# Kernel optimization log

Measured on AMD Instinct MI355X. Metric: run time of the kernel, lower is better.

## Reference

```python
import jax, jax.numpy as jnp
import numpy as np
from jax import lax

N, L, D, P, H, QK, VP = 1, 512, 256, 128, 8, 8, 8
FIN = H * P + H * VP * 7 + H * 7  # 1528: pair + value-point + beta features


def _l2g(R, t, p):
    # local_to_global: q = R @ p + t, applied over flattened point dims
    s = p.shape
    p3 = p.reshape(s[0], s[1], -1, 3)
    q = jnp.einsum('nlij,nlmj->nlmi', R, p3) + t[:, :, None, :]
    return q.reshape(s)


def _g2l(R, t, q):
    # global_to_local: p = R^T @ (q - t)
    s = q.shape
    q3 = q.reshape(s[0], s[1], -1, 3)
    p = jnp.einsum('nlji,nlmj->nlmi', R, q3 - t[:, :, None, :])
    return p.reshape(s)


def _inorm(x):  # InstanceNorm2d, affine=False, eps=1e-5, NCHW
    m = x.mean(axis=(2, 3), keepdims=True)
    v = x.var(axis=(2, 3), keepdims=True)
    return (x - m) * lax.rsqrt(v + 1e-5)


def _conv3(x, w, b):  # 3x3, stride 1, pad 1
    y = lax.conv_general_dilated(x, w, (1, 1), [(1, 1), (1, 1)],
                                 dimension_numbers=('NCHW', 'OIHW', 'NCHW'))
    return y + b[None, :, None, None]


def _ln(x, g, b):  # LayerNorm over last dim, eps=1e-5
    m = x.mean(-1, keepdims=True)
    v = x.var(-1, keepdims=True)
    return (x - m) * lax.rsqrt(v + 1e-5) * g + b


def _leaky(x):  # LeakyReLU, negative_slope=0.01
    return jnp.where(x >= 0, x, 0.01 * x)


def setup_inputs():
    key = jax.random.key(0)
    ks = jax.random.split(key, 24)
    s = 0.05
    return {
        'R': jax.random.normal(ks[0], (N, L, 3, 3), jnp.float32),
        't': jax.random.normal(ks[1], (N, L, 3), jnp.float32),
        'p_CB': jax.random.normal(ks[2], (N, L, 3), jnp.float32),
        'x': jax.random.normal(ks[3], (N, L, D), jnp.float32),
        'z': jax.random.normal(ks[4], (N, L, L, P), jnp.float32),
        'W_p2h': jax.random.normal(ks[5], (P, H), jnp.float32) * s,
        'gamma': jnp.ones((1, 1, H), jnp.float32),
        'Wq': jax.random.normal(ks[6], (D, H * QK * 3), jnp.float32) * s,
        'Wk': jax.random.normal(ks[7], (D, H * QK * 3), jnp.float32) * s,
        'Wv': jax.random.normal(ks[8], (D, H * VP * 3), jnp.float32) * s,
        'W1': jax.random.normal(ks[9], (FIN, 2 * D), jnp.float32) * s,
        'b1': jnp.zeros((2 * D,), jnp.float32),
        'ln1_g': jnp.ones((2 * D,), jnp.float32),
        'ln1_b': jnp.zeros((2 * D,), jnp.float32),
        'W2': jax.random.normal(ks[10], (2 * D, D), jnp.float32) * s,
        'b2': jnp.zeros((D,), jnp.float32),
        'ca_w': jax.random.normal(ks[11], (H, 2 * H, 3, 3), jnp.float32) * s,
        'ca_b': jnp.zeros((H,), jnp.float32),
        'ln_g': jnp.ones((D,), jnp.float32),
        'ln_b': jnp.zeros((D,), jnp.float32),
        'cp_w': jax.random.normal(ks[12], (P, H + P, 3, 3), jnp.float32) * s,
        'cp_b': jnp.zeros((P,), jnp.float32),
        'mask': jnp.ones((N, L), dtype=bool),
    }


def reference(R, t, p_CB, x, z, W_p2h, gamma, Wq, Wk, Wv, W1, b1, ln1_g, ln1_b,
              W2, b2, ca_w, ca_b, ln_g, ln_b, cp_w, cp_b, mask):
    n, l = x.shape[:2]
    # pair logits [n,l,l,H]
    logits_pair = jnp.einsum('nijp,ph->nijh', z, W_p2h)
    # spatial (point) logits: squared distances between global q/k points
    q_s = _l2g(R, t, (x @ Wq).reshape(n, l, H * QK, 3)).reshape(n, l, H, QK * 3)
    k_s = _l2g(R, t, (x @ Wk).reshape(n, l, H * QK, 3)).reshape(n, l, H, QK * 3)
    ssd = ((q_s ** 2).sum(-1)[:, :, None, :] + (k_s ** 2).sum(-1)[:, None, :, :]
           - 2.0 * jnp.einsum('nihd,njhd->nijh', q_s, k_s))
    logits_spatial = ssd * (-gamma * jnp.sqrt(2.0 / (9.0 * QK)) / 2.0)
    # conv2dalpha: InstanceNorm -> 3x3 conv -> LeakyReLU over the LxL grid
    lg = jnp.concatenate([logits_pair, logits_spatial], axis=-1).transpose(0, 3, 1, 2)
    logits_sum = _leaky(_conv3(_inorm(lg), ca_w, ca_b)).transpose(0, 2, 3, 1)
    mask_row = mask[:, :, None, None]
    mask_pair = mask_row & mask[:, None, :, None]
    logits_sum = jnp.where(mask_pair, logits_sum, logits_sum - 1e6)
    alpha = jax.nn.softmax(logits_sum, axis=2)
    alpha = jnp.where(mask_row, alpha, 0.0)
    # pair aggregation [n,l,H*P]
    feat_p2n = jnp.einsum('nijh,nijp->nihp', alpha, z).reshape(n, l, H * P)
    # spatial (value point) aggregation
    v_pts = _l2g(R, t, (x @ Wv).reshape(n, l, H, VP, 3))
    aggr = jnp.einsum('nijh,njhvc->nihvc', alpha, v_pts)
    fp = _g2l(R, t, aggr)  # [n,l,H,VP,3]
    fn = jnp.sqrt((fp ** 2).sum(-1))
    fdir = fp / (fn[..., None] + 1e-6)
    feat_spatial = jnp.concatenate(
        [fp.reshape(n, l, -1), fn.reshape(n, l, -1), fdir.reshape(n, l, -1)], -1)
    # beta (CB point) aggregation
    aggr_b = jnp.einsum('nijh,njc->nihc', alpha, p_CB)
    fpb = _g2l(R, t, aggr_b)  # [n,l,H,3]
    fnb = jnp.sqrt((fpb ** 2).sum(-1))
    fdb = fpb / (fnb[..., None] + 1e-6)
    feat_beta = jnp.concatenate([fpb.reshape(n, l, -1), fnb, fdb.reshape(n, l, -1)], -1)
    # out_transform: Linear -> LayerNorm -> LeakyReLU -> Linear
    feat_all = jnp.concatenate([feat_p2n, feat_spatial, feat_beta], -1)
    h1 = _leaky(_ln(feat_all @ W1 + b1, ln1_g, ln1_b))
    fa = h1 @ W2 + b2
    fa = jnp.where(mask[..., None], fa, 0.0)
    x_out = _ln(x + fa, ln_g, ln_b)
    # alpha2pair: InstanceNorm -> 3x3 conv -> LeakyReLU
    pz = jnp.concatenate([z, alpha], -1).transpose(0, 3, 1, 2)
    pair_out = _leaky(_conv3(_inorm(pz), cp_w, cp_b)).transpose(0, 2, 3, 1)
    return (x_out, pair_out)
```

## Files before the change

kernel.cpp:

```cpp
#include <hip/hip_runtime.h>
#include <hip/hip_bf16.h>
#include <math.h>

#define Lr 512
#define LL (512*512)
#define PZROW 73728

typedef __bf16 bf16x8 __attribute__((ext_vector_type(8)));
typedef float f32x16 __attribute__((ext_vector_type(16)));

static __device__ __forceinline__ unsigned short f2bf(float f) {
    union { float f; unsigned u; } a; a.f = f;
    unsigned r = a.u + 0x7fff + ((a.u >> 16) & 1);
    return (unsigned short)(r >> 16);
}

static __device__ __forceinline__ unsigned pack2(float lo, float hi) {
    return (unsigned)f2bf(lo) | ((unsigned)f2bf(hi) << 16);
}

__global__ __launch_bounds__(512) void zero_stats_k(float* lg_acc, float* pz_acc) {
    int t = threadIdx.x;
    if (t < 32) lg_acc[t] = 0.f;
    if (t < 272) pz_acc[t] = 0.f;
}

__global__ __launch_bounds__(256) void wb_prep_k(const float* __restrict__ cpw,
        const float* __restrict__ pzmr, unsigned short* __restrict__ wb) {
    int idx = blockIdx.x * 256 + threadIdx.x;
    if (idx >= 128 * 1296) return;
    int o = idx / 1296, k = idx % 1296;
    int tap = k / 144, c = k % 144;
    float v = (c < 136) ? cpw[(o * 136 + c) * 9 + tap] * pzmr[c * 2 + 1] : 0.f;
    wb[idx] = f2bf(v);
}

__global__ __launch_bounds__(128) void kc_prep_k(const float* __restrict__ cpw,
        const float* __restrict__ pzmr, float* __restrict__ kc) {
    int idx = blockIdx.x * 128 + threadIdx.x;
    if (idx >= 1152) return;
    int o = idx / 9, tap = idx % 9;
    float s = 0.f;
    for (int c = 0; c < 136; c++)
        s += cpw[(o * 136 + c) * 9 + tap] * pzmr[c * 2 + 1] * pzmr[c * 2];
    kc[idx] = -s;
}

__device__ __forceinline__ const float* qkv_colptr(const float* Wq, const float* Wk, const float* Wv, int c) {
    return c < 192 ? (Wq + c) : (c < 384 ? (Wk + c - 192) : (Wv + c - 384));
}

__global__ __launch_bounds__(256) void qkv_k(const float* __restrict__ x,
        const float* __restrict__ Wq, const float* __restrict__ Wk, const float* __restrict__ Wv,
        const float* __restrict__ R, const float* __restrict__ tv,
        float* __restrict__ qs, float* __restrict__ ks, float* __restrict__ vp,
        float* __restrict__ q2, float* __restrict__ k2) {
    __shared__ float xrow[256];
    __shared__ float praw[576];
    __shared__ float tr[576];
    __shared__ float Rt[12];
    int i = blockIdx.x, t = threadIdx.x;
    xrow[t] = x[i * 256 + t];
    if (t < 12) Rt[t] = (t < 9) ? R[i * 9 + t] : tv[i * 3 + t - 9];
    __syncthreads();
    const float* p0 = qkv_colptr(Wq, Wk, Wv, t);
    const float* p1 = qkv_colptr(Wq, Wk, Wv, t + 256);
    const float* p2 = qkv_colptr(Wq, Wk, Wv, t < 64 ? t + 512 : 575);
    float a0 = 0.f, a1 = 0.f, a2 = 0.f;
    for (int f = 0; f < 256; f++) {
        float xv = xrow[f];
        a0 += xv * p0[f * 192];
        a1 += xv * p1[f * 192];
        a2 += xv * p2[f * 192];
    }
    praw[t] = a0; praw[t + 256] = a1;
    if (t < 64) praw[t + 512] = a2;
    __syncthreads();
    if (t < 192) {
        int seg = t / 64, pt = t % 64;
        float b0 = praw[seg * 192 + pt * 3], b1_ = praw[seg * 192 + pt * 3 + 1], b2_ = praw[seg * 192 + pt * 3 + 2];
        #pragma unroll
        for (int r = 0; r < 3; r++)
            tr[seg * 192 + pt * 3 + r] = Rt[r * 3] * b0 + Rt[r * 3 + 1] * b1_ + Rt[r * 3 + 2] * b2_ + Rt[9 + r];
    }
    __syncthreads();
    if (t < 8) {
        float s = 0.f;
        #pragma unroll
        for (int d = 0; d < 24; d++) { float v = tr[t * 24 + d]; s += v * v; }
        q2[i * 8 + t] = s;
    } else if (t < 16) {
        int h = t - 8; float s = 0.f;
        #pragma unroll
        for (int d = 0; d < 24; d++) { float v = tr[192 + h * 24 + d]; s += v * v; }
        k2[i * 8 + h] = s;
    }
    for (int f = t; f < 576; f += 256) {
        float v = tr[f];
        if (f < 192) qs[i * 192 + f] = v;
        else if (f < 384) ks[i * 192 + f - 192] = v;
        else vp[i * 192 + f - 384] = v;
    }
}

__global__ __launch_bounds__(256) void zstats_pzb_k(const float4* __restrict__ z4,
        float* pz_acc, unsigned short* __restrict__ pzb) {
    __shared__ float acc[256];
    int t = threadIdx.x;
    acc[t] = 0.f;
    __syncthreads();
    int chunk = t & 15, pl = t >> 4;
    int p0 = blockIdx.x * 128;
    float s[8], s2[8];
    #pragma unroll
    for (int u = 0; u < 8; u++) { s[u] = 0.f; s2[u] = 0.f; }
    #pragma unroll
    for (int k = 0; k < 8; k++) {
        int pos = p0 + k * 16 + pl;
        const float4* src = z4 + (size_t)pos * 32 + chunk * 2;
        float4 v0 = src[0], v1 = src[1];
        float vv[8] = {v0.x, v0.y, v0.z, v0.w, v1.x, v1.y, v1.z, v1.w};
        #pragma unroll
        for (int u = 0; u < 8; u++) { s[u] += vv[u]; s2[u] += vv[u] * vv[u]; }
        uint4 q;
        q.x = pack2(vv[0], vv[1]); q.y = pack2(vv[2], vv[3]);
        q.z = pack2(vv[4], vv[5]); q.w = pack2(vv[6], vv[7]);
        int row = pos >> 9, col = pos & 511;
        *(uint4*)(pzb + ((size_t)row * 18 + chunk) * 4096 + col * 8) = q;
    }
    #pragma unroll
    for (int u = 0; u < 8; u++) {
        atomicAdd(&acc[(chunk * 8 + u) * 2], s[u]);
        atomicAdd(&acc[(chunk * 8 + u) * 2 + 1], s2[u]);
    }
    __syncthreads();
    if (t < 128) {
        atomicAdd(&pz_acc[t * 2], acc[t * 2]);
        atomicAdd(&pz_acc[t * 2 + 1], acc[t * 2 + 1]);
    }
}

__global__ __launch_bounds__(256) void lg_k(const float* __restrict__ z,
        const float* __restrict__ Wp2h, const float* __restrict__ gamma,
        const float* __restrict__ qs, const float* __restrict__ ks,
        const float* __restrict__ q2, const float* __restrict__ k2,
        float* __restrict__ lg, float* lg_acc) {
    __shared__ float zl[32 * 132];
    __shared__ float wh[8 * 132];
    __shared__ float qrow[192];
    __shared__ float q2row[8];
    __shared__ float sacc[32];
    int i = blockIdx.x, t = threadIdx.x;
    for (int f = t; f < 1024; f += 256) { int h = f >> 7, p = f & 127; wh[h * 132 + p] = Wp2h[p * 8 + h]; }
    if (t < 192) qrow[t] = qs[i * 192 + t];
    if (t < 8) q2row[t] = q2[i * 8 + t];
    if (t < 32) sacc[t] = 0.f;
    int jl = t >> 3, h = t & 7;
    float gsc = -gamma[h] * 0.08333333333333333f;
    float sp = 0.f, sp2 = 0.f, ss = 0.f, ss2 = 0.f;
    __syncthreads();
    for (int jt = 0; jt < 16; jt++) {
        int j0 = jt * 32;
        const float4* zsrc = (const float4*)(z + (size_t)(i * 512 + j0) * 128);
        #pragma unroll
        for (int r = 0; r < 4; r++) {
            int idx4 = r * 256 + t;
            int zjl = idx4 >> 5, p4 = idx4 & 31;
            *(float4*)&zl[zjl * 132 + p4 * 4] = zsrc[idx4];
        }
        __syncthreads();
        int j = j0 + jl;
        float accp = 0.f;
        const float4* za = (const float4*)&zl[jl * 132];
        const float4* wa = (const float4*)&wh[h * 132];
        #pragma unroll
        for (int p4 = 0; p4 < 32; p4++) {
            float4 a = za[p4], b = wa[p4];
            accp += a.x * b.x + a.y * b.y + a.z * b.z + a.w * b.w;
        }
        const float4* kp = (const float4*)(ks + (size_t)j * 192 + h * 24);
        const float4* qp = (const float4*)&qrow[h * 24];
        float dqk = 0.f;
        #pragma unroll
        for (int d4 = 0; d4 < 6; d4++) {
            float4 a = qp[d4], b = kp[d4];
            dqk += a.x * b.x + a.y * b.y + a.z * b.z + a.w * b.w;
        }
        float ssd = q2row[h] + k2[j * 8 + h] - 2.f * dqk;
        float lgs = ssd * gsc;
        lg[(size_t)h * LL + i * 512 + j] = accp;
        lg[(size_t)(8 + h) * LL + i * 512 + j] = lgs;
        sp += accp; sp2 += accp * accp; ss += lgs; ss2 += lgs * lgs;
        __syncthreads();
    }
    atomicAdd(&sacc[h * 2], sp);        atomicAdd(&sacc[h * 2 + 1], sp2);
    atomicAdd(&sacc[16 + h * 2], ss);   atomicAdd(&sacc[16 + h * 2 + 1], ss2);
    __syncthreads();
    if (t < 16) {
        atomicAdd(&lg_acc[t * 2], sacc[t * 2]);
        atomicAdd(&lg_acc[t * 2 + 1], sacc[t * 2 + 1]);
    }
}

__global__ void finalize_k(const float* __restrict__ acc, float* __restrict__ mr, int nch, float npix) {
    int t = threadIdx.x;
    if (t < nch) {
        float m = acc[t * 2] / npix;
        float v = acc[t * 2 + 1] / npix - m * m;
        mr[t * 2] = m;
        mr[t * 2 + 1] = rsqrtf(fmaxf(v, 0.f) + 1e-5f);
    }
}

__global__ __launch_bounds__(256) void ca_softmax_k(const float* __restrict__ lg,
        const float* __restrict__ lgmr, const float* __restrict__ caw, const float* __restrict__ cab,
        float* __restrict__ alpha, float* pz_acc, unsigned short* __restrict__ pzb) {
    __shared__ float wl[1152];
    __shared__ float mr[32];
    __shared__ float cb[8];
    __shared__ float red[64];
    int i = blockIdx.x, t = threadIdx.x;
    for (int f = t; f < 1152; f += 256) {
        int o = f & 7, k = f >> 3; int c = k / 9, r = k % 9;
        wl[f] = caw[(o * 16 + c) * 9 + r];
    }
    if (t < 32) mr[t] = lgmr[t];
    if (t < 8) cb[t] = cab[t];
    __syncthreads();
    float acc0[8], acc1[8];
    #pragma unroll
    for (int o = 0; o < 8; o++) { acc0[o] = 0.f; acc1[o] = 0.f; }
    int j0 = t, j1 = t + 256;
    const float4* w4 = (const float4*)wl;
    for (int c = 0; c < 16; c++) {
        float m = mr[c * 2], rs = mr[c * 2 + 1];
        const float* lgc = lg + (size_t)c * LL;
        #pragma unroll
        for (int di = 0; di < 3; di++) {
            int row = i - 1 + di;
            if (row < 0 || row >= 512) continue;
            const float* lr = lgc + (size_t)row * 512;
            float v0[3], v1[3];
            v0[0] = (j0 > 0) ? (lr[j0 - 1] - m) * rs : 0.f;
            v0[1] = (lr[j0] - m) * rs;
            v0[2] = (lr[j0 + 1] - m) * rs;
            v1[0] = (lr[j1 - 1] - m) * rs;
            v1[1] = (lr[j1] - m) * rs;
            v1[2] = (j1 < 511) ? (lr[j1 + 1] - m) * rs : 0.f;
            int wb = (c * 9 + di * 3) * 2;
            #pragma unroll
            for (int dj = 0; dj < 3; dj++) {
                float4 wa = w4[wb + dj * 2], wbv = w4[wb + dj * 2 + 1];
                acc0[0] += wa.x * v0[dj]; acc0[1] += wa.y * v0[dj]; acc0[2] += wa.z * v0[dj]; acc0[3] += wa.w * v0[dj];
                acc0[4] += wbv.x * v0[dj]; acc0[5] += wbv.y * v0[dj]; acc0[6] += wbv.z * v0[dj]; acc0[7] += wbv.w * v0[dj];
                acc1[0] += wa.x * v1[dj]; acc1[1] += wa.y * v1[dj]; acc1[2] += wa.z * v1[dj]; acc1[3] += wa.w * v1[dj];
                acc1[4] += wbv.x * v1[dj]; acc1[5] += wbv.y * v1[dj]; acc1[6] += wbv.z * v1[dj]; acc1[7] += wbv.w * v1[dj];
            }
        }
    }
    float s0[8], s1[8];
    #pragma unroll
    for (int o = 0; o < 8; o++) {
        float v = acc0[o] + cb[o]; s0[o] = v >= 0.f ? v : 0.01f * v;
        float w = acc1[o] + cb[o]; s1[o] = w >= 0.f ? w : 0.01f * w;
    }
    int lane = t & 63, wid = t >> 6;
    float mx[8];
    #pragma unroll
    for (int o = 0; o < 8; o++) mx[o] = fmaxf(s0[o], s1[o]);
    for (int off = 1; off < 64; off <<= 1) {
        #pragma unroll
        for (int o = 0; o < 8; o++) mx[o] = fmaxf(mx[o], __shfl_xor(mx[o], off));
    }
    if (lane == 0) {
        #pragma unroll
        for (int o = 0; o < 8; o++) red[wid * 8 + o] = mx[o];
    }
    __syncthreads();
    float M[8];
    #pragma unroll
    for (int o = 0; o < 8; o++) M[o] = fmaxf(fmaxf(red[o], red[8 + o]), fmaxf(red[16 + o], red[24 + o]));
    float e0[8], e1[8], sm[8];
    #pragma unroll
    for (int o = 0; o < 8; o++) { e0[o] = expf(s0[o] - M[o]); e1[o] = expf(s1[o] - M[o]); sm[o] = e0[o] + e1[o]; }
    __syncthreads();
    for (int off = 1; off < 64; off <<= 1) {
        #pragma unroll
        for (int o = 0; o < 8; o++) sm[o] += __shfl_xor(sm[o], off);
    }
    if (lane == 0) {
        #pragma unroll
        for (int o = 0; o < 8; o++) red[wid * 8 + o] = sm[o];
    }
    __syncthreads();
    float a0[8], a1[8], st_s[8], st_q[8];
    #pragma unroll
    for (int o = 0; o < 8; o++) {
        float rden = 1.f / (red[o] + red[8 + o] + red[16 + o] + red[24 + o]);
        a0[o] = e0[o] * rden; a1[o] = e1[o] * rden;
        st_s[o] = a0[o] + a1[o];
        st_q[o] = a0[o] * a0[o] + a1[o] * a1[o];
    }
    size_t base = (size_t)i * 512;
    #pragma unroll
    for (int o = 0; o < 8; o++) {
        alpha[(size_t)o * LL + base + t] = a0[o];
        alpha[(size_t)o * LL + base + t + 256] = a1[o];
    }
    {
        uint4 p0, p1;
        p0.x = pack2(a0[0], a0[1]); p0.y = pack2(a0[2], a0[3]);
        p0.z = pack2(a0[4], a0[5]); p0.w = pack2(a0[6], a0[7]);
        p1.x = pack2(a1[0], a1[1]); p1.y = pack2(a1[2], a1[3]);
        p1.z = pack2(a1[4], a1[5]); p1.w = pack2(a1[6], a1[7]);
        unsigned short* pb = pzb + (size_t)i * PZROW + 16 * 4096;
        *(uint4*)(pb + (size_t)t * 8) = p0;
        *(uint4*)(pb + (size_t)(t + 256) * 8) = p1;
        uint4 zz = {0u, 0u, 0u, 0u};
        *(uint4*)(pb + 4096 + (size_t)t * 8) = zz;
        *(uint4*)(pb + 4096 + (size_t)(t + 256) * 8) = zz;
    }
    __syncthreads();
    for (int off = 1; off < 64; off <<= 1) {
        #pragma unroll
        for (int o = 0; o < 8; o++) { st_s[o] += __shfl_xor(st_s[o], off); st_q[o] += __shfl_xor(st_q[o], off); }
    }
    if (lane == 0) {
        #pragma unroll
        for (int o = 0; o < 8; o++) { red[wid * 8 + o] = st_s[o]; red[32 + wid * 8 + o] = st_q[o]; }
    }
    __syncthreads();
    if (t < 8) {
        float ts = red[t] + red[8 + t] + red[16 + t] + red[24 + t];
        float tq = red[32 + t] + red[40 + t] + red[48 + t] + red[56 + t];
        atomicAdd(&pz_acc[(128 + t) * 2], ts);
        atomicAdd(&pz_acc[(128 + t) * 2 + 1], tq);
    }
}

__global__ __launch_bounds__(256) void feat_mlp_k(
        const float* __restrict__ alpha, const float* __restrict__ z,
        const float* __restrict__ vp, const float* __restrict__ pcb,
        const float* __restrict__ R, const float* __restrict__ tv,
        const float* __restrict__ W1, const float* __restrict__ b1,
        const float* __restrict__ ln1g, const float* __restrict__ ln1b,
        const float* __restrict__ W2, const float* __restrict__ b2,
        const float* __restrict__ lng, const float* __restrict__ lnb,
        const float* __restrict__ x, float* __restrict__ xout) {
    __shared__ float al[8 * 512];
    __shared__ float zl[64 * 128];
    __shared__ float feat[1536];
    __shared__ float h1[512];
    __shared__ float agg[216];
    __shared__ float Rt[12];
    __shared__ float redl[8];
    int i = blockIdx.x, t = threadIdx.x;
    for (int f = t; f < 4096; f += 256) al[f] = alpha[(size_t)(f >> 9) * LL + i * 512 + (f & 511)];
    if (t < 12) Rt[t] = (t < 9) ? R[i * 9 + t] : tv[i * 3 + t - 9];
    __syncthreads();
    if (t < 216) {
        float a = 0.f;
        if (t < 192) {
            int h = t / 24;
            const float* vptr = vp + t;
            const float* ar = al + h * 512;
            for (int j = 0; j < 512; j++) a += ar[j] * vptr[(size_t)j * 192];
        } else {
            int u = t - 192; int h = u / 3, cc = u % 3;
            const float* ar = al + h * 512;
            for (int j = 0; j < 512; j++) a += ar[j] * pcb[j * 3 + cc];
        }
        agg[t] = a;
    }
    float4 accp = {0.f, 0.f, 0.f, 0.f};
    int hh = t >> 5, p4 = t & 31;
    for (int jc = 0; jc < 8; jc++) {
        const float4* zsrc = (const float4*)(z + (size_t)(i * 512 + jc * 64) * 128);
        #pragma unroll
        for (int r = 0; r < 8; r++) ((float4*)zl)[r * 256 + t] = zsrc[r * 256 + t];
        __syncthreads();
        const float* ar = al + hh * 512 + jc * 64;
        const float4* zv = (const float4*)zl + p4;
        #pragma unroll 4
        for (int jl = 0; jl < 64; jl++) {
            float a = ar[jl];
            float4 v = zv[jl * 32];
            accp.x += a * v.x; accp.y += a * v.y; accp.z += a * v.z; accp.w += a * v.w;
        }
        __syncthreads();
    }
    *(float4*)&feat[hh * 128 + p4 * 4] = accp;
    __syncthreads();
    if (t < 64) {
        int h = t >> 3, v = t & 7;
        float d0 = agg[h * 24 + v * 3] - Rt[9];
        float d1 = agg[h * 24 + v * 3 + 1] - Rt[10];
        float d2 = agg[h * 24 + v * 3 + 2] - Rt[11];
        float f0 = Rt[0] * d0 + Rt[3] * d1 + Rt[6] * d2;
        float f1 = Rt[1] * d0 + Rt[4] * d1 + Rt[7] * d2;
        float f2 = Rt[2] * d0 + Rt[5] * d1 + Rt[8] * d2;
        float n = sqrtf(f0 * f0 + f1 * f1 + f2 * f2);
        float rn = 1.f / (n + 1e-6f);
        feat[1024 + h * 24 + v * 3] = f0;
        feat[1024 + h * 24 + v * 3 + 1] = f1;
        feat[1024 + h * 24 + v * 3 + 2] = f2;
        feat[1216 + h * 8 + v] = n;
        feat[1280 + h * 24 + v * 3] = f0 * rn;
        feat[1280 + h * 24 + v * 3 + 1] = f1 * rn;
        feat[1280 + h * 24 + v * 3 + 2] = f2 * rn;
    } else if (t < 72) {
        int h = t - 64;
        float d0 = agg[192 + h * 3] - Rt[9];
        float d1 = agg[192 + h * 3 + 1] - Rt[10];
        float d2 = agg[192 + h * 3 + 2] - Rt[11];
        float f0 = Rt[0] * d0 + Rt[3] * d1 + Rt[6] * d2;
        float f1 = Rt[1] * d0 + Rt[4] * d1 + Rt[7] * d2;
        float f2 = Rt[2] * d0 + Rt[5] * d1 + Rt[8] * d2;
        float n = sqrtf(f0 * f0 + f1 * f1 + f2 * f2);
        float rn = 1.f / (n + 1e-6f);
        feat[1472 + h * 3] = f0; feat[1472 + h * 3 + 1] = f1; feat[1472 + h * 3 + 2] = f2;
        feat[1496 + h] = n;
        feat[1504 + h * 3] = f0 * rn; feat[1504 + h * 3 + 1] = f1 * rn; feat[1504 + h * 3 + 2] = f2 * rn;
    }
    __syncthreads();
    float acc0 = b1[t], acc1 = b1[t + 256];
    const float4* f4 = (const float4*)feat;
    for (int f = 0; f < 1528; f += 4) {
        float4 fv = f4[f >> 2];
        const float* w = W1 + (size_t)f * 512 + t;
        acc0 += fv.x * w[0] + fv.y * w[512] + fv.z * w[1024] + fv.w * w[1536];
        const float* w2p = w + 256;
        acc1 += fv.x * w2p[0] + fv.y * w2p[512] + fv.z * w2p[1024] + fv.w * w2p[1536];
    }
    int lane = t & 63, wid = t >> 6;
    float s = acc0 + acc1, s2 = acc0 * acc0 + acc1 * acc1;
    for (int off = 1; off < 64; off <<= 1) { s += __shfl_xor(s, off); s2 += __shfl_xor(s2, off); }
    if (lane == 0) { redl[wid * 2] = s; redl[wid * 2 + 1] = s2; }
    __syncthreads();
    float S = redl[0] + redl[2] + redl[4] + redl[6];
    float S2 = redl[1] + redl[3] + redl[5] + redl[7];
    float mean = S / 512.f;
    float rstd = rsqrtf(fmaxf(S2 / 512.f - mean * mean, 0.f) + 1e-5f);
    float hv0 = (acc0 - mean) * rstd * ln1g[t] + ln1b[t];
    float hv1 = (acc1 - mean) * rstd * ln1g[t + 256] + ln1b[t + 256];
    hv0 = hv0 >= 0.f ? hv0 : 0.01f * hv0;
    hv1 = hv1 >= 0.f ? hv1 : 0.01f * hv1;
    h1[t] = hv0; h1[t + 256] = hv1;
    __syncthreads();
    float a2 = b2[t];
    const float4* h14 = (const float4*)h1;
    for (int k = 0; k < 512; k += 4) {
        float4 hv = h14[k >> 2];
        const float* w = W2 + (size_t)k * 256 + t;
        a2 += hv.x * w[0] + hv.y * w[256] + hv.z * w[512] + hv.w * w[768];
    }
    float xv = x[i * 256 + t] + a2;
    float ss_ = xv, sq_ = xv * xv;
    for (int off = 1; off < 64; off <<= 1) { ss_ += __shfl_xor(ss_, off); sq_ += __shfl_xor(sq_, off); }
    __syncthreads();
    if (lane == 0) { redl[wid * 2] = ss_; redl[wid * 2 + 1] = sq_; }
    __syncthreads();
    float Sx = redl[0] + redl[2] + redl[4] + redl[6];
    float Sx2 = redl[1] + redl[3] + redl[5] + redl[7];
    float mx = Sx / 256.f;
    float rsx = rsqrtf(fmaxf(Sx2 / 256.f - mx * mx, 0.f) + 1e-5f);
    xout[i * 256 + t] = (xv - mx) * rsx * lng[t] + lnb[t];
}

__global__ __launch_bounds__(256) void conv_mfma_k(
        const unsigned short* __restrict__ pzb, const unsigned short* __restrict__ wb,
        const float* __restrict__ kc, const float* __restrict__ cpb,
        float* __restrict__ pout) {
    __shared__ unsigned short abuf[2368 * 8];
    __shared__ float csA[128];
    __shared__ float cs0[128];
    __shared__ float cs2[128];
    int t = threadIdx.x;
    int bid = blockIdx.x;
    int swz = (bid & 7) * 256 + (bid >> 3);
    int i = swz >> 2;
    int j0 = (swz & 3) * 128;
    if (t < 128) {
        int o = t;
        float a0 = 0.f, a1 = 0.f, a2 = 0.f;
        #pragma unroll
        for (int di = 0; di < 3; di++) {
            int grow = i - 1 + di;
            if (grow < 0 || grow > 511) continue;
            a0 += kc[o * 9 + di * 3];
            a1 += kc[o * 9 + di * 3 + 1];
            a2 += kc[o * 9 + di * 3 + 2];
        }
        cs0[o] = a0; cs2[o] = a2; csA[o] = cpb[o] + a0 + a1 + a2;
    }
    int w = t >> 6, lane = t & 63;
    int l31 = lane & 31, lhi = lane >> 5;
    int mt0 = (w & 1) * 64;
    int nt0 = (w >> 1) * 64;

    uint4 rg[10];
    #define STAGE_LOAD(DI) do {                                                \
        int grow_ = i - 1 + (DI);                                              \
        bool rowok_ = (grow_ >= 0 && grow_ < 512);                             \
        const unsigned short* rowp_ = pzb + (size_t)grow_ * PZROW;             \
        _Pragma("unroll")                                                      \
        for (int k = 0; k < 10; k++) {                                         \
            int f_ = t + k * 256;                                              \
            uint4 v_ = {0u, 0u, 0u, 0u};                                       \
            if (f_ < 2340) {                                                   \
                int c_ = f_ / 130, col_ = f_ - c_ * 130;                       \
                int gcol_ = j0 - 1 + col_;                                     \
                if (rowok_ && (unsigned)gcol_ < 512u)                          \
                    v_ = *(const uint4*)(rowp_ + c_ * 4096 + gcol_ * 8);       \
            }                                                                  \
            rg[k] = v_;                                                        \
        }                                                                      \
    } while (0)

    #define STAGE_WRITE() do {                                                 \
        _Pragma("unroll")                                                      \
        for (int k = 0; k < 10; k++) {                                         \
            int f_ = t + k * 256;                                              \
            if (f_ < 2340) *(uint4*)(abuf + f_ * 8) = rg[k];                   \
        }                                                                      \
    } while (0)

    f32x16 acc00 = {}, acc01 = {}, acc10 = {}, acc11 = {};

    STAGE_LOAD(0);
    STAGE_WRITE();
    __syncthreads();

    #pragma unroll
    for (int di = 0; di < 3; di++) {
        if (di < 2) STAGE_LOAD(di + 1);
        #pragma unroll
        for (int dj = 0; dj < 3; dj++) {
            int tap = di * 3 + dj;
            const unsigned short* wp0 = wb + (size_t)(nt0 + l31) * 1296 + tap * 144 + lhi * 8;
            const unsigned short* wp1 = wp0 + 32 * 1296;
            const unsigned short* ap0 = abuf + lhi * 1040 + (mt0 + l31 + dj) * 8;
            const unsigned short* ap1 = ap0 + 256;
            #pragma unroll
            for (int ksn = 0; ksn < 9; ksn++) {
                bf16x8 a0 = *(const bf16x8*)(ap0 + ksn * 2080);
                bf16x8 a1 = *(const bf16x8*)(ap1 + ksn * 2080);
                bf16x8 b0 = *(const bf16x8*)(wp0 + ksn * 16);
                bf16x8 b1 = *(const bf16x8*)(wp1 + ksn * 16);
                acc00 = __builtin_amdgcn_mfma_f32_32x32x16_bf16(a0, b0, acc00, 0, 0, 0);
                acc01 = __builtin_amdgcn_mfma_f32_32x32x16_bf16(a0, b1, acc01, 0, 0, 0);
                acc10 = __builtin_amdgcn_mfma_f32_32x32x16_bf16(a1, b0, acc10, 0, 0, 0);
                acc11 = __builtin_amdgcn_mfma_f32_32x32x16_bf16(a1, b1, acc11, 0, 0, 0);
            }
        }
        __syncthreads();
        if (di < 2) {
            STAGE_WRITE();
            __syncthreads();
        }
    }
    #undef STAGE_LOAD
    #undef STAGE_WRITE

    #pragma unroll
    for (int mi = 0; mi < 2; mi++) {
        #pragma unroll
        for (int ni = 0; ni < 2; ni++) {
            const f32x16* a = (mi == 0) ? (ni == 0 ? &acc00 : &acc01) : (ni == 0 ? &acc10 : &acc11);
            int nb = nt0 + ni * 32 + l31;
            float bA = csA[nb], b0_ = cs0[nb], b2_ = cs2[nb];
            #pragma unroll
            for (int r = 0; r < 16; r++) {
                int m = mt0 + mi * 32 + 4 * lhi + (r & 3) + 8 * (r >> 2);
                int j = j0 + m;
                float bias = bA - (j == 0 ? b0_ : 0.f) - (j == 511 ? b2_ : 0.f);
                float v = (*a)[r] + bias;
                v = v >= 0.f ? v : 0.01f * v;
                pout[((size_t)(i * 512 + j)) * 128 + nb] = v;
            }
        }
    }
}

extern "C" void kernel_launch(void* const* d_in, const int* in_sizes, int n_in,
                              void* d_out, int out_size, void* d_ws, size_t ws_size,
                              hipStream_t stream) {
    (void)in_sizes; (void)n_in; (void)out_size; (void)ws_size;
    const float* R    = (const float*)d_in[0];
    const float* tv   = (const float*)d_in[1];
    const float* pcb  = (const float*)d_in[2];
    const float* x    = (const float*)d_in[3];
    const float* z    = (const float*)d_in[4];
    const float* wp2h = (const float*)d_in[5];
    const float* gamma= (const float*)d_in[6];
    const float* Wq   = (const float*)d_in[7];
    const float* Wk   = (const float*)d_in[8];
    const float* Wv   = (const float*)d_in[9];
    const float* W1   = (const float*)d_in[10];
    const float* b1   = (const float*)d_in[11];
    const float* ln1g = (const float*)d_in[12];
    const float* ln1b = (const float*)d_in[13];
    const float* W2   = (const float*)d_in[14];
    const float* b2   = (const float*)d_in[15];
    const float* caw  = (const float*)d_in[16];
    const float* cab  = (const float*)d_in[17];
    const float* lng  = (const float*)d_in[18];
    const float* lnb  = (const float*)d_in[19];
    const float* cpw  = (const float*)d_in[20];
    const float* cpb  = (const float*)d_in[21];

    float* ws = (float*)d_ws;
    float* qs     = ws;
    float* ksv    = qs + 98304;
    float* vp     = ksv + 98304;
    float* q2     = vp + 98304;
    float* k2     = q2 + 4096;
    float* lg_acc = k2 + 4096;
    float* lg_mr  = lg_acc + 32;
    float* pz_acc = lg_mr + 32;
    float* pz_mr  = pz_acc + 272;
    float* kc     = pz_mr + 272;
    unsigned short* wbq = (unsigned short*)(kc + 1152);
    float* lg     = kc + 1152 + 82944;
    float* alpha  = lg + 16 * LL;
    unsigned short* pzb = (unsigned short*)(alpha + 8 * LL);

    float* xout = (float*)d_out;
    float* pout = xout + 131072;

    hipLaunchKernelGGL(zero_stats_k, dim3(1), dim3(512), 0, stream, lg_acc, pz_acc);
    hipLaunchKernelGGL(qkv_k, dim3(512), dim3(256), 0, stream, x, Wq, Wk, Wv, R, tv, qs, ksv, vp, q2, k2);
    hipLaunchKernelGGL(zstats_pzb_k, dim3(2048), dim3(256), 0, stream, (const float4*)z, pz_acc, pzb);
    hipLaunchKernelGGL(lg_k, dim3(512), dim3(256), 0, stream, z, wp2h, gamma, qs, ksv, q2, k2, lg, lg_acc);
    hipLaunchKernelGGL(finalize_k, dim3(1), dim3(64), 0, stream, lg_acc, lg_mr, 16, 262144.f);
    hipLaunchKernelGGL(ca_softmax_k, dim3(512), dim3(256), 0, stream, lg, lg_mr, caw, cab, alpha, pz_acc, pzb);
    hipLaunchKernelGGL(finalize_k, dim3(1), dim3(192), 0, stream, pz_acc, pz_mr, 136, 262144.f);
    hipLaunchKernelGGL(wb_prep_k, dim3(648), dim3(256), 0, stream, cpw, pz_mr, wbq);
    hipLaunchKernelGGL(kc_prep_k, dim3(9), dim3(128), 0, stream, cpw, pz_mr, kc);
    hipLaunchKernelGGL(feat_mlp_k, dim3(512), dim3(256), 0, stream,
                       alpha, z, vp, pcb, R, tv, W1, b1, ln1g, ln1b, W2, b2, lng, lnb, x, xout);
    hipLaunchKernelGGL(conv_mfma_k, dim3(2048), dim3(256), 0, stream, pzb, wbq, kc, cpb, pout);
}
```

Baseline: 775.0 us.

## Split feature aggregation from MLP, transpose value points, stage conv output stores

Measured after the change: 827.9 us. 1.07x slower.

```diff
diff --git a/kernel.cpp b/kernel.cpp
--- a/kernel.cpp
+++ b/kernel.cpp
@@ -19,10 +19,14 @@
     return (unsigned)f2bf(lo) | ((unsigned)f2bf(hi) << 16);
 }
 
-__global__ __launch_bounds__(512) void zero_stats_k(float* lg_acc, float* pz_acc) {
-    int t = threadIdx.x;
-    if (t < 32) lg_acc[t] = 0.f;
-    if (t < 272) pz_acc[t] = 0.f;
+__global__ __launch_bounds__(512) void zero_stats_k(float* lg_acc, float* pz_acc,
+        float* vpT, const float* __restrict__ pcb) {
+    int t = threadIdx.x, b = blockIdx.x;
+    if (b == 0) {
+        if (t < 32) lg_acc[t] = 0.f;
+        if (t < 272) pz_acc[t] = 0.f;
+    }
+    vpT[(size_t)(192 + b) * 512 + t] = pcb[t * 3 + b];
 }
 
 __global__ __launch_bounds__(256) void wb_prep_k(const float* __restrict__ cpw,
@@ -53,7 +57,7 @@
 __global__ __launch_bounds__(256) void qkv_k(const float* __restrict__ x,
         const float* __restrict__ Wq, const float* __restrict__ Wk, const float* __restrict__ Wv,
         const float* __restrict__ R, const float* __restrict__ tv,
-        float* __restrict__ qs, float* __restrict__ ks, float* __restrict__ vp,
+        float* __restrict__ qs, float* __restrict__ ks, float* __restrict__ vpT,
         float* __restrict__ q2, float* __restrict__ k2) {
     __shared__ float xrow[256];
     __shared__ float praw[576];
@@ -95,12 +99,12 @@
         for (int d = 0; d < 24; d++) { float v = tr[192 + h * 24 + d]; s += v * v; }
         k2[i * 8 + h] = s;
     }
-    for (int f = t; f < 576; f += 256) {
+    for (int f = t; f < 384; f += 256) {
         float v = tr[f];
         if (f < 192) qs[i * 192 + f] = v;
-        else if (f < 384) ks[i * 192 + f - 192] = v;
-        else vp[i * 192 + f - 384] = v;
-    }
+        else ks[i * 192 + f - 192] = v;
+    }
+    if (t < 192) vpT[(size_t)t * 512 + i] = tr[384 + t];
 }
 
 __global__ __launch_bounds__(256) void zstats_pzb_k(const float4* __restrict__ z4,
@@ -338,58 +342,61 @@
     }
 }
 
-__global__ __launch_bounds__(256) void feat_mlp_k(
+__global__ __launch_bounds__(256) void aggfeat_k(
         const float* __restrict__ alpha, const float* __restrict__ z,
-        const float* __restrict__ vp, const float* __restrict__ pcb,
+        const float* __restrict__ vpT,
         const float* __restrict__ R, const float* __restrict__ tv,
-        const float* __restrict__ W1, const float* __restrict__ b1,
-        const float* __restrict__ ln1g, const float* __restrict__ ln1b,
-        const float* __restrict__ W2, const float* __restrict__ b2,
-        const float* __restrict__ lng, const float* __restrict__ lnb,
-        const float* __restrict__ x, float* __restrict__ xout) {
+        float* __restrict__ featg) {
     __shared__ float al[8 * 512];
-    __shared__ float zl[64 * 128];
-    __shared__ float feat[1536];
-    __shared__ float h1[512];
+    __shared__ float zl[32 * 128];
     __shared__ float agg[216];
+    __shared__ float featl[512];
     __shared__ float Rt[12];
-    __shared__ float redl[8];
     int i = blockIdx.x, t = threadIdx.x;
-    for (int f = t; f < 4096; f += 256) al[f] = alpha[(size_t)(f >> 9) * LL + i * 512 + (f & 511)];
+    float4 rg[4];
+    const float4* zsrc = (const float4*)(z + (size_t)i * 512 * 128);
+    #pragma unroll
+    for (int k = 0; k < 4; k++) rg[k] = zsrc[k * 256 + t];
+    #pragma unroll
+    for (int f = t; f < 1024; f += 256)
+        ((float4*)al)[f] = ((const float4*)(alpha + (size_t)(f >> 7) * LL + (size_t)i * 512))[f & 127];
     if (t < 12) Rt[t] = (t < 9) ? R[i * 9 + t] : tv[i * 3 + t - 9];
-    __syncthreads();
-    if (t < 216) {
-        float a = 0.f;
-        if (t < 192) {
-            int h = t / 24;
-            const float* vptr = vp + t;
-            const float* ar = al + h * 512;
-            for (int j = 0; j < 512; j++) a += ar[j] * vptr[(size_t)j * 192];
-        } else {
-            int u = t - 192; int h = u / 3, cc = u % 3;
-            const float* ar = al + h * 512;
-            for (int j = 0; j < 512; j++) a += ar[j] * pcb[j * 3 + cc];
-        }
-        agg[t] = a;
-    }
+    int hh = t >> 5, p4 = t & 31;
     float4 accp = {0.f, 0.f, 0.f, 0.f};
-    int hh = t >> 5, p4 = t & 31;
-    for (int jc = 0; jc < 8; jc++) {
-        const float4* zsrc = (const float4*)(z + (size_t)(i * 512 + jc * 64) * 128);
-        #pragma unroll
-        for (int r = 0; r < 8; r++) ((float4*)zl)[r * 256 + t] = zsrc[r * 256 + t];
+    for (int jc = 0; jc < 16; jc++) {
+        #pragma unroll
+        for (int k = 0; k < 4; k++) ((float4*)zl)[k * 256 + t] = rg[k];
         __syncthreads();
-        const float* ar = al + hh * 512 + jc * 64;
+        if (jc < 15) {
+            const float4* zn = zsrc + (size_t)(jc + 1) * 1024;
+            #pragma unroll
+            for (int k = 0; k < 4; k++) rg[k] = zn[k * 256 + t];
+        }
+        const float* ar = al + hh * 512 + jc * 32;
         const float4* zv = (const float4*)zl + p4;
-        #pragma unroll 4
-        for (int jl = 0; jl < 64; jl++) {
+        #pragma unroll 8
+        for (int jl = 0; jl < 32; jl++) {
             float a = ar[jl];
             float4 v = zv[jl * 32];
             accp.x += a * v.x; accp.y += a * v.y; accp.z += a * v.z; accp.w += a * v.w;
         }
         __syncthreads();
     }
-    *(float4*)&feat[hh * 128 + p4 * 4] = accp;
+    *(float4*)(featg + (size_t)i * 1536 + t * 4) = accp;
+    if (t < 216) {
+        const float* src; int h;
+        if (t < 192) { src = vpT + (size_t)t * 512; h = t / 24; }
+        else { int u = t - 192; src = vpT + (size_t)(192 + u % 3) * 512; h = u / 3; }
+        const float4* s4 = (const float4*)src;
+        const float4* a4 = (const float4*)(al + h * 512);
+        float acc = 0.f;
+        #pragma unroll 8
+        for (int k = 0; k < 128; k++) {
+            float4 a = a4[k], b = s4[k];
+            acc += a.x * b.x + a.y * b.y + a.z * b.z + a.w * b.w;
+        }
+        agg[t] = acc;
+    }
     __syncthreads();
     if (t < 64) {
         int h = t >> 3, v = t & 7;
@@ -401,13 +408,13 @@
         float f2 = Rt[2] * d0 + Rt[5] * d1 + Rt[8] * d2;
         float n = sqrtf(f0 * f0 + f1 * f1 + f2 * f2);
         float rn = 1.f / (n + 1e-6f);
-        feat[1024 + h * 24 + v * 3] = f0;
-        feat[1024 + h * 24 + v * 3 + 1] = f1;
-        feat[1024 + h * 24 + v * 3 + 2] = f2;
-        feat[1216 + h * 8 + v] = n;
-        feat[1280 + h * 24 + v * 3] = f0 * rn;
-        feat[1280 + h * 24 + v * 3 + 1] = f1 * rn;
-        feat[1280 + h * 24 + v * 3 + 2] = f2 * rn;
+        featl[h * 24 + v * 3] = f0;
+        featl[h * 24 + v * 3 + 1] = f1;
+        featl[h * 24 + v * 3 + 2] = f2;
+        featl[192 + h * 8 + v] = n;
+        featl[256 + h * 24 + v * 3] = f0 * rn;
+        featl[256 + h * 24 + v * 3 + 1] = f1 * rn;
+        featl[256 + h * 24 + v * 3 + 2] = f2 * rn;
     } else if (t < 72) {
         int h = t - 64;
         float d0 = agg[192 + h * 3] - Rt[9];
@@ -418,53 +425,92 @@
         float f2 = Rt[2] * d0 + Rt[5] * d1 + Rt[8] * d2;
         float n = sqrtf(f0 * f0 + f1 * f1 + f2 * f2);
         float rn = 1.f / (n + 1e-6f);
-        feat[1472 + h * 3] = f0; feat[1472 + h * 3 + 1] = f1; feat[1472 + h * 3 + 2] = f2;
-        feat[1496 + h] = n;
-        feat[1504 + h * 3] = f0 * rn; feat[1504 + h * 3 + 1] = f1 * rn; feat[1504 + h * 3 + 2] = f2 * rn;
-    }
-    __syncthreads();
-    float acc0 = b1[t], acc1 = b1[t + 256];
-    const float4* f4 = (const float4*)feat;
-    for (int f = 0; f < 1528; f += 4) {
-        float4 fv = f4[f >> 2];
-        const float* w = W1 + (size_t)f * 512 + t;
-        acc0 += fv.x * w[0] + fv.y * w[512] + fv.z * w[1024] + fv.w * w[1536];
-        const float* w2p = w + 256;
-        acc1 += fv.x * w2p[0] + fv.y * w2p[512] + fv.z * w2p[1024] + fv.w * w2p[1536];
+        featl[448 + h * 3] = f0; featl[448 + h * 3 + 1] = f1; featl[448 + h * 3 + 2] = f2;
+        featl[472 + h] = n;
+        featl[480 + h * 3] = f0 * rn; featl[480 + h * 3 + 1] = f1 * rn; featl[480 + h * 3 + 2] = f2 * rn;
+    } else if (t < 80) {
+        featl[432 + t] = 0.f;
+    }
+    __syncthreads();
+    if (t < 128)
+        ((float4*)(featg + (size_t)i * 1536 + 1024))[t] = ((const float4*)featl)[t];
+}
+
+__global__ __launch_bounds__(256) void mlp_k(
+        const float* __restrict__ featg,
+        const float* __restrict__ W1, const float* __restrict__ b1,
+        const float* __restrict__ ln1g, const float* __restrict__ ln1b,
+        const float* __restrict__ W2, const float* __restrict__ b2,
+        const float* __restrict__ lng, const float* __restrict__ lnb,
+        const float* __restrict__ x, float* __restrict__ xout) {
+    __shared__ float fl[2][1528];
+    __shared__ float h1[2][512];
+    __shared__ float red[16];
+    int b = blockIdx.x, t = threadIdx.x;
+    int i0 = b * 2;
+    for (int f = t; f < 764; f += 256) {
+        int r = f / 382, k = f - r * 382;
+        ((float4*)fl[r])[k] = ((const float4*)(featg + (size_t)(i0 + r) * 1536))[k];
+    }
+    __syncthreads();
+    float a00 = b1[t], a01 = b1[t + 256];
+    float a10 = a00, a11 = a01;
+    for (int k = 0; k < 1528; k += 4) {
+        float4 f0 = *(const float4*)&fl[0][k];
+        float4 f1 = *(const float4*)&fl[1][k];
+        const float* w = W1 + (size_t)k * 512 + t;
+        float w0 = w[0], w1 = w[512], w2 = w[1024], w3 = w[1536];
+        float v0 = w[256], v1 = w[768], v2 = w[1280], v3 = w[1792];
+        a00 += f0.x * w0 + f0.y * w1 + f0.z * w2 + f0.w * w3;
+        a01 += f0.x * v0 + f0.y * v1 + f0.z * v2 + f0.w * v3;
+        a10 += f1.x * w0 + f1.y * w1 + f1.z * w2 + f1.w * w3;
+        a11 += f1.x * v0 + f1.y * v1 + f1.z * v2 + f1.w * v3;
     }
     int lane = t & 63, wid = t >> 6;
-    float s = acc0 + acc1, s2 = acc0 * acc0 + acc1 * acc1;
-    for (int off = 1; off < 64; off <<= 1) { s += __shfl_xor(s, off); s2 += __shfl_xor(s2, off); }
-    if (lane == 0) { redl[wid * 2] = s; redl[wid * 2 + 1] = s2; }
-    __syncthreads();
-    float S = redl[0] + redl[2] + redl[4] + redl[6];
-    float S2 = redl[1] + redl[3] + redl[5] + redl[7];
-    float mean = S / 512.f;
-    float rstd = rsqrtf(fmaxf(S2 / 512.f - mean * mean, 0.f) + 1e-5f);
-    float hv0 = (acc0 - mean) * rstd * ln1g[t] + ln1b[t];
-    float hv1 = (acc1 - mean) * rstd * ln1g[t + 256] + ln1b[t + 256];
-    hv0 = hv0 >= 0.f ? hv0 : 0.01f * hv0;
-    hv1 = hv1 >= 0.f ? hv1 : 0.01f * hv1;
-    h1[t] = hv0; h1[t + 256] = hv1;
-    __syncthreads();
-    float a2 = b2[t];
-    const float4* h14 = (const float4*)h1;
+    float s0 = a00 + a01, q0 = a00 * a00 + a01 * a01;
+    float s1 = a10 + a11, q1 = a10 * a10 + a11 * a11;
+    for (int off = 1; off < 64; off <<= 1) {
+        s0 += __shfl_xor(s0, off); q0 += __shfl_xor(q0, off);
+        s1 += __shfl_xor(s1, off); q1 += __shfl_xor(q1, off);
+    }
+    if (lane == 0) { red[wid * 4] = s0; red[wid * 4 + 1] = q0; red[wid * 4 + 2] = s1; red[wid * 4 + 3] = q1; }
+    __syncthreads();
+    float S0 = red[0] + red[4] + red[8] + red[12], Q0 = red[1] + red[5] + red[9] + red[13];
+    float S1 = red[2] + red[6] + red[10] + red[14], Q1 = red[3] + red[7] + red[11] + red[15];
+    float m0 = S0 / 512.f, r0 = rsqrtf(fmaxf(Q0 / 512.f - m0 * m0, 0.f) + 1e-5f);
+    float m1 = S1 / 512.f, r1 = rsqrtf(fmaxf(Q1 / 512.f - m1 * m1, 0.f) + 1e-5f);
+    float g0 = ln1g[t], g1 = ln1g[t + 256], bb0 = ln1b[t], bb1 = ln1b[t + 256];
+    float h00 = (a00 - m0) * r0 * g0 + bb0; h00 = h00 >= 0.f ? h00 : 0.01f * h00;
+    float h01 = (a01 - m0) * r0 * g1 + bb1; h01 = h01 >= 0.f ? h01 : 0.01f * h01;
+    float h10 = (a10 - m1) * r1 * g0 + bb0; h10 = h10 >= 0.f ? h10 : 0.01f * h10;
+    float h11 = (a11 - m1) * r1 * g1 + bb1; h11 = h11 >= 0.f ? h11 : 0.01f * h11;
+    h1[0][t] = h00; h1[0][t + 256] = h01; h1[1][t] = h10; h1[1][t + 256] = h11;
+    __syncthreads();
+    float c0 = b2[t], c1 = c0;
     for (int k = 0; k < 512; k += 4) {
-        float4 hv = h14[k >> 2];
+        float4 hv0 = *(const float4*)&h1[0][k];
+        float4 hv1 = *(const float4*)&h1[1][k];
         const float* w = W2 + (size_t)k * 256 + t;
-        a2 += hv.x * w[0] + hv.y * w[256] + hv.z * w[512] + hv.w * w[768];
-    }
-    float xv = x[i * 256 + t] + a2;
-    float ss_ = xv, sq_ = xv * xv;
-    for (int off = 1; off < 64; off <<= 1) { ss_ += __shfl_xor(ss_, off); sq_ += __shfl_xor(sq_, off); }
-    __syncthreads();
-    if (lane == 0) { redl[wid * 2] = ss_; redl[wid * 2 + 1] = sq_; }
-    __syncthreads();
-    float Sx = redl[0] + redl[2] + redl[4] + redl[6];
-    float Sx2 = redl[1] + redl[3] + redl[5] + redl[7];
-    float mx = Sx / 256.f;
-    float rsx = rsqrtf(fmaxf(Sx2 / 256.f - mx * mx, 0.f) + 1e-5f);
-    xout[i * 256 + t] = (xv - mx) * rsx * lng[t] + lnb[t];
+        float w0 = w[0], w1 = w[256], w2 = w[512], w3 = w[768];
+        c0 += hv0.x * w0 + hv0.y * w1 + hv0.z * w2 + hv0.w * w3;
+        c1 += hv1.x * w0 + hv1.y * w1 + hv1.z * w2 + hv1.w * w3;
+    }
+    float xv0 = x[(size_t)i0 * 256 + t] + c0;
+    float xv1 = x[(size_t)(i0 + 1) * 256 + t] + c1;
+    float ss0 = xv0, qq0 = xv0 * xv0, ss1 = xv1, qq1 = xv1 * xv1;
+    for (int off = 1; off < 64; off <<= 1) {
+        ss0 += __shfl_xor(ss0, off); qq0 += __shfl_xor(qq0, off);
+        ss1 += __shfl_xor(ss1, off); qq1 += __shfl_xor(qq1, off);
+    }
+    __syncthreads();
+    if (lane == 0) { red[wid * 4] = ss0; red[wid * 4 + 1] = qq0; red[wid * 4 + 2] = ss1; red[wid * 4 + 3] = qq1; }
+    __syncthreads();
+    float Sx0 = red[0] + red[4] + red[8] + red[12], Qx0 = red[1] + red[5] + red[9] + red[13];
+    float Sx1 = red[2] + red[6] + red[10] + red[14], Qx1 = red[3] + red[7] + red[11] + red[15];
+    float mx0 = Sx0 / 256.f, rx0 = rsqrtf(fmaxf(Qx0 / 256.f - mx0 * mx0, 0.f) + 1e-5f);
+    float mx1 = Sx1 / 256.f, rx1 = rsqrtf(fmaxf(Qx1 / 256.f - mx1 * mx1, 0.f) + 1e-5f);
+    xout[(size_t)i0 * 256 + t] = (xv0 - mx0) * rx0 * lng[t] + lnb[t];
+    xout[(size_t)(i0 + 1) * 256 + t] = (xv1 - mx1) * rx1 * lng[t] + lnb[t];
 }
 
 __global__ __launch_bounds__(256) void conv_mfma_k(
@@ -562,23 +608,38 @@
     #undef STAGE_LOAD
     #undef STAGE_WRITE
 
-    #pragma unroll
-    for (int mi = 0; mi < 2; mi++) {
-        #pragma unroll
-        for (int ni = 0; ni < 2; ni++) {
-            const f32x16* a = (mi == 0) ? (ni == 0 ? &acc00 : &acc01) : (ni == 0 ? &acc10 : &acc11);
-            int nb = nt0 + ni * 32 + l31;
-            float bA = csA[nb], b0_ = cs0[nb], b2_ = cs2[nb];
+    float* fb = (float*)abuf;
+    #pragma unroll
+    for (int mh = 0; mh < 2; mh++) {
+        if ((w & 1) == mh) {
             #pragma unroll
-            for (int r = 0; r < 16; r++) {
-                int m = mt0 + mi * 32 + 4 * lhi + (r & 3) + 8 * (r >> 2);
-                int j = j0 + m;
-                float bias = bA - (j == 0 ? b0_ : 0.f) - (j == 511 ? b2_ : 0.f);
-                float v = (*a)[r] + bias;
-                v = v >= 0.f ? v : 0.01f * v;
-                pout[((size_t)(i * 512 + j)) * 128 + nb] = v;
+            for (int mi = 0; mi < 2; mi++) {
+                #pragma unroll
+                for (int ni = 0; ni < 2; ni++) {
+                    const f32x16* a = (mi == 0) ? (ni == 0 ? &acc00 : &acc01) : (ni == 0 ? &acc10 : &acc11);
+                    int nb = nt0 + ni * 32 + l31;
+                    float bA = csA[nb], b0_ = cs0[nb], b2_ = cs2[nb];
+                    #pragma unroll
+                    for (int r = 0; r < 16; r++) {
+                        int ml = mi * 32 + 4 * lhi + (r & 3) + 8 * (r >> 2);
+                        int j = j0 + mh * 64 + ml;
+                        float bias = bA - (j == 0 ? b0_ : 0.f) - (j == 511 ? b2_ : 0.f);
+                        float v = (*a)[r] + bias;
+                        v = v >= 0.f ? v : 0.01f * v;
+                        fb[ml * 128 + nb] = v;
+                    }
+                }
             }
         }
+        __syncthreads();
+        const float4* fb4 = (const float4*)fb;
+        float4* gdst = (float4*)(pout + ((size_t)(i * 512 + j0 + mh * 64)) * 128);
+        #pragma unroll
+        for (int k = 0; k < 8; k++) {
+            int f4i = k * 256 + t;
+            gdst[f4i] = fb4[f4i];
+        }
+        __syncthreads();
     }
 }
 
@@ -612,8 +673,8 @@
     float* ws = (float*)d_ws;
     float* qs     = ws;
     float* ksv    = qs + 98304;
-    float* vp     = ksv + 98304;
-    float* q2     = vp + 98304;
+    float* vpT    = ksv + 98304;
+    float* q2     = vpT + 100352;
     float* k2     = q2 + 4096;
     float* lg_acc = k2 + 4096;
     float* lg_mr  = lg_acc + 32;
@@ -621,15 +682,16 @@
     float* pz_mr  = pz_acc + 272;
     float* kc     = pz_mr + 272;
     unsigned short* wbq = (unsigned short*)(kc + 1152);
-    float* lg     = kc + 1152 + 82944;
+    float* featg  = kc + 1152 + 82944;
+    float* lg     = featg + 786432;
     float* alpha  = lg + 16 * LL;
     unsigned short* pzb = (unsigned short*)(alpha + 8 * LL);
 
     float* xout = (float*)d_out;
     float* pout = xout + 131072;
 
-    hipLaunchKernelGGL(zero_stats_k, dim3(1), dim3(512), 0, stream, lg_acc, pz_acc);
-    hipLaunchKernelGGL(qkv_k, dim3(512), dim3(256), 0, stream, x, Wq, Wk, Wv, R, tv, qs, ksv, vp, q2, k2);
+    hipLaunchKernelGGL(zero_stats_k, dim3(3), dim3(512), 0, stream, lg_acc, pz_acc, vpT, pcb);
+    hipLaunchKernelGGL(qkv_k, dim3(512), dim3(256), 0, stream, x, Wq, Wk, Wv, R, tv, qs, ksv, vpT, q2, k2);
     hipLaunchKernelGGL(zstats_pzb_k, dim3(2048), dim3(256), 0, stream, (const float4*)z, pz_acc, pzb);
     hipLaunchKernelGGL(lg_k, dim3(512), dim3(256), 0, stream, z, wp2h, gamma, qs, ksv, q2, k2, lg, lg_acc);
     hipLaunchKernelGGL(finalize_k, dim3(1), dim3(64), 0, stream, lg_acc, lg_mr, 16, 262144.f);
@@ -637,7 +699,8 @@
     hipLaunchKernelGGL(finalize_k, dim3(1), dim3(192), 0, stream, pz_acc, pz_mr, 136, 262144.f);
     hipLaunchKernelGGL(wb_prep_k, dim3(648), dim3(256), 0, stream, cpw, pz_mr, wbq);
     hipLaunchKernelGGL(kc_prep_k, dim3(9), dim3(128), 0, stream, cpw, pz_mr, kc);
-    hipLaunchKernelGGL(feat_mlp_k, dim3(512), dim3(256), 0, stream,
-                       alpha, z, vp, pcb, R, tv, W1, b1, ln1g, ln1b, W2, b2, lng, lnb, x, xout);
+    hipLaunchKernelGGL(aggfeat_k, dim3(512), dim3(256), 0, stream, alpha, z, vpT, R, tv, featg);
+    hipLaunchKernelGGL(mlp_k, dim3(256), dim3(256), 0, stream,
+                       featg, W1, b1, ln1g, ln1b, W2, b2, lng, lnb, x, xout);
     hipLaunchKernelGGL(conv_mfma_k, dim3(2048), dim3(256), 0, stream, pzb, wbq, kc, cpb, pout);
 }
```
